# Performance work log

Hardware: AMD Instinct MI355X
Metric: run time of the kernel (lower is better)

The kernel has to match this reference:

```python
import jax, jax.numpy as jnp
from jax import lax
import numpy as np

B, T, D, H, P = 2048, 256, 128, 256, 2048


def setup_inputs() -> dict:
    key = jax.random.key(0)
    ks = jax.random.split(key, 6)
    s_ih = 1.0 / np.sqrt(H)  # PyTorch GRU init scale
    return {
        "x": jax.random.normal(ks[0], (B, T, D), dtype=jnp.float32),
        "w_ih": jax.random.uniform(ks[1], (3 * H, D), minval=-s_ih, maxval=s_ih, dtype=jnp.float32),
        "w_hh": jax.random.uniform(ks[2], (3 * H, H), minval=-s_ih, maxval=s_ih, dtype=jnp.float32),
        "b_ih": jax.random.uniform(ks[3], (3 * H,), minval=-s_ih, maxval=s_ih, dtype=jnp.float32),
        "b_hh": jax.random.uniform(ks[4], (3 * H,), minval=-s_ih, maxval=s_ih, dtype=jnp.float32),
        "prototypes": jax.random.normal(ks[5], (P, H), dtype=jnp.float32),
    }


def _gru_last_hidden(x, w_ih, w_hh, b_ih, b_hh):
    # Precompute all input projections in one big GEMM: [B, T, 3H]
    x_proj = jnp.einsum("btd,gd->btg", x, w_ih) + b_ih
    h0 = jnp.zeros((x.shape[0], w_hh.shape[1]), x.dtype)

    def step(h, xp):
        hp = h @ w_hh.T + b_hh                       # [B, 3H]
        xr, xz, xn = jnp.split(xp, 3, axis=-1)       # gate order: r, z, n (PyTorch)
        hr, hz, hn = jnp.split(hp, 3, axis=-1)
        r = jax.nn.sigmoid(xr + hr)
        z = jax.nn.sigmoid(xz + hz)
        n = jnp.tanh(xn + r * hn)
        h = (1.0 - z) * n + z * h
        return h, None

    h_last, _ = lax.scan(step, h0, jnp.swapaxes(x_proj, 0, 1))  # scan over time
    return h_last  # [B, H]


def _cdist(h, prototypes):
    # Euclidean distance via ||h||^2 + ||p||^2 - 2 h.p^T (same math as torch.cdist p=2)
    d2 = (
        jnp.sum(h * h, axis=1, keepdims=True)
        + jnp.sum(prototypes * prototypes, axis=1)
        - 2.0 * (h @ prototypes.T)
    )
    return jnp.sqrt(jnp.maximum(d2, 0.0))  # [B, P]


def reference(x, w_ih, w_hh, b_ih, b_hh, prototypes):
    h_last = _gru_last_hidden(x, w_ih, w_hh, b_ih, b_hh)
    dists = _cdist(h_last, prototypes)
    assignments = jnp.argmin(dists, axis=1)  # [B] int
    return assignments
```

## Files before the change

### kernel.cpp

```cpp
#include <hip/hip_runtime.h>

#define TT 256
#define DD 128
#define HH 256
#define PP 2048
#define RB 16
#define NBLK 128
#define NTH 1024

typedef _Float16 half8 __attribute__((ext_vector_type(8)));
typedef _Float16 half4 __attribute__((ext_vector_type(4)));
typedef float f32x4 __attribute__((ext_vector_type(4)));

#define MFMA16(a, b, c) __builtin_amdgcn_mfma_f32_16x16x32_f16((a), (b), (c), 0, 0, 0)
#define INV2048 (4.8828125e-4f)

__device__ __forceinline__ float fast_sigmoid(float v) {
    return __builtin_amdgcn_rcpf(1.0f + __expf(-v));
}
__device__ __forceinline__ float fast_tanh(float v) {
    const float e2 = __expf(2.0f * v);
    return 1.0f - 2.0f * __builtin_amdgcn_rcpf(e2 + 1.0f);
}

__global__ void prep_kernel(const float* __restrict__ w_ih, const float* __restrict__ w_hh,
                            const float* __restrict__ protos,
                            _Float16* __restrict__ WF, float* __restrict__ pT) {
    int f = blockIdx.x * blockDim.x + threadIdx.x;
    if (f < 294912) {
        int s = f / 24576, rem = f % 24576;
        int tt = rem / 512, rem2 = rem % 512;
        int m = rem2 >> 5, kl = rem2 & 31;
        int grow = (tt % 3) * 256 + (tt / 3) * 16 + m;
        float v = (s < 4) ? w_ih[grow * DD + s * 32 + kl]
                          : w_hh[grow * HH + (s - 4) * 32 + kl];
        _Float16 hi = (_Float16)v;
        _Float16 lo = (_Float16)((v - (float)hi) * 2048.0f);
        int lane = m + 16 * (kl >> 3);
        int base = ((s * 2 + 0) * 48 + tt) * 512 + lane * 8 + (kl & 7);
        WF[base] = hi;
        WF[base + 48 * 512] = lo;
    }
    if (f < HH * PP) pT[f] = protos[(f & (PP - 1)) * HH + (f >> 11)];
}

__launch_bounds__(NTH)
__global__ void gru_kernel(const float* __restrict__ x,
                           const _Float16* __restrict__ WF,
                           const float* __restrict__ b_ih, const float* __restrict__ b_hh,
                           const float* __restrict__ pT,
                           int* __restrict__ out) {
    __shared__ __align__(16) _Float16 fragB[2 * 24 * 512];
    __shared__ float hsF[HH * RB];
    __shared__ float redv[16][RB];
    __shared__ int   redi[16][RB];
#define FRAG(b, sec) (fragB + ((b) * 24 + (sec)) * 512)

    const int tid  = threadIdx.x;
    const int lane = tid & 63;
    const int w    = tid >> 6;
    const int row0 = blockIdx.x * RB;
    const int lane8 = lane * 8;
    const int t0w   = 3 * w;
    const int sw    = (w >= 12) ? (w - 12) : w;

    float bRv[4], bZv[4], bXNv[4], bHNv[4];
    #pragma unroll
    for (int r = 0; r < 4; ++r) {
        const int j = 16 * w + ((lane >> 4) << 2) + r;
        bRv[r]  = b_ih[j] + b_hh[j];
        bZv[r]  = b_ih[HH + j] + b_hh[HH + j];
        bXNv[r] = b_ih[2 * HH + j];
        bHNv[r] = b_hh[2 * HH + j];
    }

    float hprev[4] = {0.f, 0.f, 0.f, 0.f};

    const int xn = tid >> 5, xk0 = (tid & 31) * 4;
    const float* const xrow = x + (size_t)(row0 + (xn & 15)) * TT * DD + xk0;
    const int xsec = 2 * (xk0 >> 5);
    const int xidx = (((xk0 & 31) >> 3) * 16 + (xn & 15)) * 8 + (xk0 & 7);

    if (tid < 512) {
        const float4 v = *(const float4*)xrow;
        const float vv[4] = {v.x, v.y, v.z, v.w};
        _Float16 xh[4], xl[4];
        #pragma unroll
        for (int u = 0; u < 4; ++u) {
            xh[u] = (_Float16)vv[u];
            xl[u] = (_Float16)((vv[u] - (float)xh[u]) * 2048.0f);
        }
        *(half4*)(FRAG(0, xsec) + xidx)     = half4{xh[0], xh[1], xh[2], xh[3]};
        *(half4*)(FRAG(0, xsec + 1) + xidx) = half4{xl[0], xl[1], xl[2], xl[3]};
        _Float16* hz = FRAG(0, 8);
        const half8 z8 = {};
        *(half8*)(hz + tid * 16)     = z8;
        *(half8*)(hz + tid * 16 + 8) = z8;
    }
    __syncthreads();

    const half8* __restrict__ WH = (const half8*)WF;

    for (int t = 0; t < TT; ++t) {
        const int cur = t & 1, nxtb = cur ^ 1;

        float4 pfx = make_float4(0.f, 0.f, 0.f, 0.f);
        const bool havepf = (t + 1 < TT) && (tid < 512);
        if (havepf) pfx = *(const float4*)(xrow + (size_t)(t + 1) * DD);

        f32x4 aM[3], aX[3], aMh, aXh;
        #pragma unroll
        for (int i = 0; i < 3; ++i) { aM[i] = f32x4{0.f,0.f,0.f,0.f}; aX[i] = f32x4{0.f,0.f,0.f,0.f}; }
        aMh = f32x4{0.f,0.f,0.f,0.f}; aXh = f32x4{0.f,0.f,0.f,0.f};

        #pragma unroll 2
        for (int i = 0; i < 12; ++i) {
            int s = sw + i; if (s >= 12) s -= 12;
            const half8 bh = *(const half8*)(FRAG(cur, 2 * s) + lane8);
            const half8 bl = *(const half8*)(FRAG(cur, 2 * s + 1) + lane8);
            const bool isX = (s < 4);
            #pragma unroll
            for (int i2 = 0; i2 < 3; ++i2) {
                const half8 wh = WH[((2 * s) * 48 + t0w + i2) * 64 + lane];
                const half8 wl = WH[((2 * s + 1) * 48 + t0w + i2) * 64 + lane];
                if (i2 == 2 && !isX) {
                    aMh = MFMA16(wh, bh, aMh);
                    aXh = MFMA16(wh, bl, aXh);
                    aXh = MFMA16(wl, bh, aXh);
                } else {
                    aM[i2] = MFMA16(wh, bh, aM[i2]);
                    aX[i2] = MFMA16(wh, bl, aX[i2]);
                    aX[i2] = MFMA16(wl, bh, aX[i2]);
                }
            }
        }

        {
            _Float16 hh_[4], hl_[4];
            #pragma unroll
            for (int r = 0; r < 4; ++r) {
                const float sR  = aM[0][r] + aX[0][r] * INV2048 + bRv[r];
                const float sZ  = aM[1][r] + aX[1][r] * INV2048 + bZv[r];
                const float sXN = aM[2][r] + aX[2][r] * INV2048 + bXNv[r];
                const float sHN = aMh[r]   + aXh[r]   * INV2048 + bHNv[r];
                const float Rg = fast_sigmoid(sR);
                const float Zg = fast_sigmoid(sZ);
                const float Ng = fast_tanh(sXN + Rg * sHN);
                const float h = (1.0f - Zg) * Ng + Zg * hprev[r];
                hprev[r] = h;
                hh_[r] = (_Float16)h;
                hl_[r] = (_Float16)((h - (float)hh_[r]) * 2048.0f);
            }
            const int jb  = 16 * w + ((lane >> 4) << 2);
            const int sec = 2 * (4 + (jb >> 5));
            const int idx = (((jb & 31) >> 3) * 16 + (lane & 15)) * 8 + (jb & 7);
            *(half4*)(FRAG(nxtb, sec) + idx)     = half4{hh_[0], hh_[1], hh_[2], hh_[3]};
            *(half4*)(FRAG(nxtb, sec + 1) + idx) = half4{hl_[0], hl_[1], hl_[2], hl_[3]};
        }

        if (havepf) {
            const float vv[4] = {pfx.x, pfx.y, pfx.z, pfx.w};
            _Float16 xh[4], xl[4];
            #pragma unroll
            for (int u = 0; u < 4; ++u) {
                xh[u] = (_Float16)vv[u];
                xl[u] = (_Float16)((vv[u] - (float)xh[u]) * 2048.0f);
            }
            *(half4*)(FRAG(nxtb, xsec) + xidx)     = half4{xh[0], xh[1], xh[2], xh[3]};
            *(half4*)(FRAG(nxtb, xsec + 1) + xidx) = half4{xl[0], xl[1], xl[2], xl[3]};
        }
        __syncthreads();
    }

    #pragma unroll
    for (int r = 0; r < 4; ++r) {
        const int j = 16 * w + ((lane >> 4) << 2) + r;
        hsF[j * RB + (lane & 15)] = hprev[r];
    }
    __syncthreads();

    float bv[16]; int bi[16];
    #pragma unroll
    for (int r = 0; r < 16; ++r) { bv[r] = 3.4e38f; bi[r] = 0; }
    for (int m = 0; m < 2; ++m) {
        const int p = m * 1024 + tid;
        float d2[16];
        #pragma unroll
        for (int r = 0; r < 16; ++r) d2[r] = 0.f;
        #pragma unroll 2
        for (int k = 0; k < HH; ++k) {
            const float pv = pT[(size_t)k * PP + p];
            #pragma unroll
            for (int g4 = 0; g4 < 4; ++g4) {
                const float4 hv = *(const float4*)&hsF[k * RB + g4 * 4];
                float d;
                d = hv.x - pv; d2[g4 * 4 + 0] += d * d;
                d = hv.y - pv; d2[g4 * 4 + 1] += d * d;
                d = hv.z - pv; d2[g4 * 4 + 2] += d * d;
                d = hv.w - pv; d2[g4 * 4 + 3] += d * d;
            }
        }
        #pragma unroll
        for (int r = 0; r < 16; ++r)
            if (d2[r] < bv[r]) { bv[r] = d2[r]; bi[r] = p; }
    }
    #pragma unroll
    for (int s = 1; s < 64; s <<= 1) {
        #pragma unroll
        for (int r = 0; r < 16; ++r) {
            const float ov = __shfl_xor(bv[r], s);
            const int   oi = __shfl_xor(bi[r], s);
            if (ov < bv[r] || (ov == bv[r] && oi < bi[r])) { bv[r] = ov; bi[r] = oi; }
        }
    }
    if (lane == 0) {
        #pragma unroll
        for (int r = 0; r < 16; ++r) { redv[w][r] = bv[r]; redi[w][r] = bi[r]; }
    }
    __syncthreads();
    if (tid < RB) {
        float v = redv[0][tid]; int idx = redi[0][tid];
        #pragma unroll
        for (int u = 1; u < 16; ++u) {
            const float ov = redv[u][tid]; const int oi = redi[u][tid];
            if (ov < v || (ov == v && oi < idx)) { v = ov; idx = oi; }
        }
        out[row0 + tid] = idx;
    }
}

extern "C" void kernel_launch(void* const* d_in, const int* in_sizes, int n_in,
                              void* d_out, int out_size, void* d_ws, size_t ws_size,
                              hipStream_t stream) {
    const float* x      = (const float*)d_in[0];
    const float* w_ih   = (const float*)d_in[1];
    const float* w_hh   = (const float*)d_in[2];
    const float* b_ih   = (const float*)d_in[3];
    const float* b_hh   = (const float*)d_in[4];
    const float* protos = (const float*)d_in[5];
    int* out = (int*)d_out;

    _Float16* WF = (_Float16*)d_ws;
    float*    pT = (float*)((char*)d_ws + 589824 * sizeof(_Float16));

    hipLaunchKernelGGL(prep_kernel, dim3((HH * PP + 255) / 256), dim3(256), 0, stream,
                       w_ih, w_hh, protos, WF, pT);
    hipLaunchKernelGGL(gru_kernel, dim3(NBLK), dim3(NTH), 0, stream,
                       x, WF, b_ih, b_hh, pT, out);
}
```

Before: 2.477 ms.

## Pin first three weight K-slices in registers and LDS across timesteps

Slices 0-1 of the fused hi/lo fp16 weight fragments are loaded once into registers, and slice 2 is copied into a large shared-memory buffer. The recurrent loop reads these from registers and LDS instead of reloading them from global memory every timestep. The remaining nine slices still stream through a rotated loop with adjusted indexing. In exchange it adds about 48 VGPRs per thread under a 1024-thread launch bound, which risks spills. It also enlarges LDS to about 144 KB by overlaying the pinned weights on the buffer later used for hidden states and reductions.

```diff
diff --git a/kernel.cpp b/kernel.cpp
--- a/kernel.cpp
+++ b/kernel.cpp
@@ -50,10 +50,12 @@
                            const float* __restrict__ b_ih, const float* __restrict__ b_hh,
                            const float* __restrict__ pT,
                            int* __restrict__ out) {
-    __shared__ __align__(16) _Float16 fragB[2 * 24 * 512];
-    __shared__ float hsF[HH * RB];
-    __shared__ float redv[16][RB];
-    __shared__ int   redi[16][RB];
+    __shared__ __align__(16) unsigned char smem[147456];
+    _Float16* const fragB = (_Float16*)smem;
+    _Float16* const pinL  = (_Float16*)(smem + 49152);
+    float* const hsF      = (float*)(smem + 49152);
+    float (*redv)[RB]     = (float (*)[RB])(smem + 49152 + 16384);
+    int   (*redi)[RB]     = (int   (*)[RB])(smem + 49152 + 16384 + 1024);
 #define FRAG(b, sec) (fragB + ((b) * 24 + (sec)) * 512)
 
     const int tid  = threadIdx.x;
@@ -62,7 +64,7 @@
     const int row0 = blockIdx.x * RB;
     const int lane8 = lane * 8;
     const int t0w   = 3 * w;
-    const int sw    = (w >= 12) ? (w - 12) : w;
+    const int sw    = (w >= 9) ? (w - 9) : w;
 
     float bRv[4], bZv[4], bXNv[4], bHNv[4];
     #pragma unroll
@@ -76,6 +78,28 @@
 
     float hprev[4] = {0.f, 0.f, 0.f, 0.f};
 
+    const half8* __restrict__ WH = (const half8*)WF;
+
+    const half8 w0h0 = WH[(0 * 48 + t0w + 0) * 64 + lane];
+    const half8 w0h1 = WH[(0 * 48 + t0w + 1) * 64 + lane];
+    const half8 w0h2 = WH[(0 * 48 + t0w + 2) * 64 + lane];
+    const half8 w0l0 = WH[(1 * 48 + t0w + 0) * 64 + lane];
+    const half8 w0l1 = WH[(1 * 48 + t0w + 1) * 64 + lane];
+    const half8 w0l2 = WH[(1 * 48 + t0w + 2) * 64 + lane];
+    const half8 w1h0 = WH[(2 * 48 + t0w + 0) * 64 + lane];
+    const half8 w1h1 = WH[(2 * 48 + t0w + 1) * 64 + lane];
+    const half8 w1h2 = WH[(2 * 48 + t0w + 2) * 64 + lane];
+    const half8 w1l0 = WH[(3 * 48 + t0w + 0) * 64 + lane];
+    const half8 w1l1 = WH[(3 * 48 + t0w + 1) * 64 + lane];
+    const half8 w1l2 = WH[(3 * 48 + t0w + 2) * 64 + lane];
+
+    {
+        const half8* src = (const half8*)(WF + 4 * 48 * 512);
+        #pragma unroll
+        for (int u = 0; u < 6; ++u)
+            *(half8*)(pinL + (u * NTH + tid) * 8) = src[u * NTH + tid];
+    }
+
     const int xn = tid >> 5, xk0 = (tid & 31) * 4;
     const float* const xrow = x + (size_t)(row0 + (xn & 15)) * TT * DD + xk0;
     const int xsec = 2 * (xk0 >> 5);
@@ -99,8 +123,6 @@
     }
     __syncthreads();
 
-    const half8* __restrict__ WH = (const half8*)WF;
-
     for (int t = 0; t < TT; ++t) {
         const int cur = t & 1, nxtb = cur ^ 1;
 
@@ -113,9 +135,36 @@
         for (int i = 0; i < 3; ++i) { aM[i] = f32x4{0.f,0.f,0.f,0.f}; aX[i] = f32x4{0.f,0.f,0.f,0.f}; }
         aMh = f32x4{0.f,0.f,0.f,0.f}; aXh = f32x4{0.f,0.f,0.f,0.f};
 
-        #pragma unroll 2
-        for (int i = 0; i < 12; ++i) {
-            int s = sw + i; if (s >= 12) s -= 12;
+        {
+            const half8 bh = *(const half8*)(FRAG(cur, 0) + lane8);
+            const half8 bl = *(const half8*)(FRAG(cur, 1) + lane8);
+            aM[0] = MFMA16(w0h0, bh, aM[0]); aX[0] = MFMA16(w0h0, bl, aX[0]); aX[0] = MFMA16(w0l0, bh, aX[0]);
+            aM[1] = MFMA16(w0h1, bh, aM[1]); aX[1] = MFMA16(w0h1, bl, aX[1]); aX[1] = MFMA16(w0l1, bh, aX[1]);
+            aM[2] = MFMA16(w0h2, bh, aM[2]); aX[2] = MFMA16(w0h2, bl, aX[2]); aX[2] = MFMA16(w0l2, bh, aX[2]);
+        }
+        {
+            const half8 bh = *(const half8*)(FRAG(cur, 2) + lane8);
+            const half8 bl = *(const half8*)(FRAG(cur, 3) + lane8);
+            aM[0] = MFMA16(w1h0, bh, aM[0]); aX[0] = MFMA16(w1h0, bl, aX[0]); aX[0] = MFMA16(w1l0, bh, aX[0]);
+            aM[1] = MFMA16(w1h1, bh, aM[1]); aX[1] = MFMA16(w1h1, bl, aX[1]); aX[1] = MFMA16(w1l1, bh, aX[1]);
+            aM[2] = MFMA16(w1h2, bh, aM[2]); aX[2] = MFMA16(w1h2, bl, aX[2]); aX[2] = MFMA16(w1l2, bh, aX[2]);
+        }
+        {
+            const half8 bh = *(const half8*)(FRAG(cur, 4) + lane8);
+            const half8 bl = *(const half8*)(FRAG(cur, 5) + lane8);
+            #pragma unroll
+            for (int i = 0; i < 3; ++i) {
+                const half8 wh = *(const half8*)(pinL + ((0 * 48 + t0w + i) << 9) + lane8);
+                const half8 wl = *(const half8*)(pinL + ((1 * 48 + t0w + i) << 9) + lane8);
+                aM[i] = MFMA16(wh, bh, aM[i]);
+                aX[i] = MFMA16(wh, bl, aX[i]);
+                aX[i] = MFMA16(wl, bh, aX[i]);
+            }
+        }
+
+        #pragma unroll 3
+        for (int i = 0; i < 9; ++i) {
+            int s = 3 + sw + i; if (s >= 12) s -= 9;
             const half8 bh = *(const half8*)(FRAG(cur, 2 * s) + lane8);
             const half8 bl = *(const half8*)(FRAG(cur, 2 * s + 1) + lane8);
             const bool isX = (s < 4);
```

Measured after the change: 2.716 ms. 1.1x slower.
